# Kernel optimization log

Hardware: AMD Instinct MI355X
Metric: run time of the kernel (lower is better)

## Reference

```python
import jax, jax.numpy as jnp
import numpy as np

EMBED = 2560
HEADS = 8
HEAD_DIM = EMBED // HEADS

def setup_inputs() -> dict:
    key = jax.random.key(0)
    k1, k2, k3, k4, k5 = jax.random.split(key, 5)
    x = jax.random.normal(k1, (2, 2048, EMBED), dtype=jnp.float32)
    # nn.Linear(embed, 3*embed): weight [3E, E], bias [3E]
    s = 1.0 / np.sqrt(EMBED)
    W_qkv = jax.random.uniform(k2, (3 * EMBED, EMBED), jnp.float32, -s, s)
    b_qkv = jax.random.uniform(k3, (3 * EMBED,), jnp.float32, -s, s)
    W_out = jax.random.uniform(k4, (EMBED, EMBED), jnp.float32, -s, s)
    b_out = jax.random.uniform(k5, (EMBED,), jnp.float32, -s, s)
    return {"x": x, "W_qkv": W_qkv, "b_qkv": b_qkv, "W_out": W_out, "b_out": b_out}

def reference(x, W_qkv, b_qkv, W_out, b_out):
    N, S, E = x.shape
    qkv = jnp.einsum('bse,fe->bsf', x, W_qkv) + b_qkv            # [B,S,3E]
    qkv = qkv.reshape(N, S, 3, HEADS, HEAD_DIM)
    q = jnp.transpose(qkv[:, :, 0], (0, 2, 1, 3))                 # [B,H,S,D]
    k = jnp.transpose(qkv[:, :, 1], (0, 2, 1, 3))
    v = jnp.transpose(qkv[:, :, 2], (0, 2, 1, 3))
    scale = jnp.sqrt(jnp.float32(HEAD_DIM))
    attn = jnp.einsum('bhqd,bhkd->bhqk', q, k) / scale            # [B,H,S,S]
    attn = jax.nn.softmax(attn, axis=-1)
    out = jnp.einsum('bhqk,bhkd->bhqd', attn, v)                  # [B,H,S,D]
    out = jnp.transpose(out, (0, 2, 1, 3)).reshape(N, S, E)
    return jnp.einsum('bse,fe->bsf', out, W_out) + b_out
```

## Files before the change

kernel.cpp:

```cpp
#include <hip/hip_runtime.h>

#define EMBED 2560
#define HEADS 8
#define HDIM  320
#define BATCH 2
#define SEQ   2048
#define MTOT  (BATCH*SEQ)
#define FTOT  (3*EMBED)

using bf = __bf16;
typedef __bf16 bf16x8 __attribute__((ext_vector_type(8)));
typedef float  f32x4  __attribute__((ext_vector_type(4)));
typedef short  s16x8  __attribute__((ext_vector_type(8)));
typedef float  f32x4v __attribute__((ext_vector_type(4)));

__device__ __forceinline__ void gl_lds16(const bf* g, bf* l) {
    __builtin_amdgcn_global_load_lds(
        (const __attribute__((address_space(1))) void*)g,
        (__attribute__((address_space(3))) void*)l,
        16, 0, 0);
}

__global__ void cvt_bf16(const float* __restrict__ in, bf* __restrict__ out, int n) {
    int i = (blockIdx.x*blockDim.x + threadIdx.x)*8;
    if (i >= n) return;
    f32x4v a = *reinterpret_cast<const f32x4v*>(in + i);
    f32x4v b = *reinterpret_cast<const f32x4v*>(in + i + 4);
    bf16x8 r;
    r[0]=(bf)a[0]; r[1]=(bf)a[1]; r[2]=(bf)a[2]; r[3]=(bf)a[3];
    r[4]=(bf)b[0]; r[5]=(bf)b[1]; r[6]=(bf)b[2]; r[7]=(bf)b[3];
    *reinterpret_cast<bf16x8*>(out + i) = r;
}

template<bool OUTBF>
__global__ __launch_bounds__(512, 2)
void gemm256(const bf* __restrict__ A, const bf* __restrict__ B,
             const float* __restrict__ bias, void* __restrict__ Cp,
             int M, int N, int K) {
    __shared__ __align__(16) bf AsL[2][2][8192];
    __shared__ __align__(16) bf BsL[2][2][8192];
    const int tid = threadIdx.x, lane = tid & 63, wid = tid >> 6;
    const int wr = wid >> 2, wc = wid & 3;
    const int l15 = lane & 15, l4 = lane >> 4;

    int mb, nb;
    const int i = blockIdx.y*gridDim.x + blockIdx.x;
    if ((gridDim.y == 16) && ((gridDim.x & 1) == 0)) {
        const int xcd = i & 7, j = i >> 3;
        const int pc = xcd & 1, pr = xcd >> 1;
        nb = pc*(gridDim.x >> 1) + (j >> 2);
        mb = pr*4 + (j & 3);
    } else {
        const int nwg = gridDim.x*gridDim.y;
        int bid = ((nwg & 7) == 0) ? (i & 7)*(nwg >> 3) + (i >> 3) : i;
        mb = bid / gridDim.x; nb = bid % gridDim.x;
    }
    const int m0 = mb*256, n0 = nb*256;
    const int NT = K >> 6;

    unsigned aOff[2];
    #pragma unroll
    for (int j = 0; j < 2; ++j) {
        int q = (wid*2 + j)*64 + lane;
        int r = q >> 3, c = q & 7;
        aOff[j] = (unsigned)r*K + (unsigned)((c ^ (r & 7))*8);
    }
    const bf* Ap = A + (size_t)m0*K;
    const bf* Bp = B + (size_t)n0*K;

    auto stA = [&](int bb, int h, int kt) {
        bf* d = &AsL[bb][h][wid*1024];
        const bf* s = Ap + (size_t)h*128*K + (size_t)kt*64;
        gl_lds16(s + aOff[0], d);
        gl_lds16(s + aOff[1], d + 512);
    };
    auto stB = [&](int bb, int h, int kt) {
        bf* d = &BsL[bb][h][wid*1024];
        const bf* s = Bp + (size_t)h*128*K + (size_t)kt*64;
        gl_lds16(s + aOff[0], d);
        gl_lds16(s + aOff[1], d + 512);
    };

    f32x4 acc[8][4] = {};
    bf16x8 aR[4][2], bR0[2][2], bR1[2][2];

    stB(0,0,0); stB(0,1,0); stA(0,0,0); stA(0,1,0); stB(1,0,1); stB(1,1,1);
    asm volatile("s_waitcnt vmcnt(4)" ::: "memory");
    __builtin_amdgcn_s_barrier();

    const int brow0 = (wc & 1)*64;
    for (int kt = 0; kt < NT; ++kt) {
        const int bb = kt & 1;
        const bf* Ab = &AsL[bb][wr][0];
        const bf* Bb = &BsL[bb][wc >> 1][0];

        #pragma unroll
        for (int mi = 0; mi < 4; ++mi)
            #pragma unroll
            for (int kk = 0; kk < 2; ++kk) {
                int r = mi*16 + l15;
                int kg = kk*4 + l4;
                aR[mi][kk] = *reinterpret_cast<const bf16x8*>(&Ab[r*64 + ((kg ^ (r & 7))*8)]);
            }
        #pragma unroll
        for (int ni = 0; ni < 2; ++ni)
            #pragma unroll
            for (int kk = 0; kk < 2; ++kk) {
                int r = brow0 + ni*16 + l15;
                int kg = kk*4 + l4;
                bR0[ni][kk] = *reinterpret_cast<const bf16x8*>(&Bb[r*64 + ((kg ^ (r & 7))*8)]);
            }
        if (kt + 1 < NT) stA(bb^1, 0, kt+1);
        __builtin_amdgcn_s_barrier();
        asm volatile("s_waitcnt lgkmcnt(0)" ::: "memory");
        __builtin_amdgcn_sched_barrier(0);
        __builtin_amdgcn_s_setprio(1);
        #pragma unroll
        for (int mi = 0; mi < 4; ++mi)
            #pragma unroll
            for (int ni = 0; ni < 2; ++ni)
                #pragma unroll
                for (int kk = 0; kk < 2; ++kk)
                    acc[mi][ni] = __builtin_amdgcn_mfma_f32_16x16x32_bf16(aR[mi][kk], bR0[ni][kk], acc[mi][ni], 0, 0, 0);
        __builtin_amdgcn_s_setprio(0);
        __builtin_amdgcn_s_barrier();

        #pragma unroll
        for (int ni = 0; ni < 2; ++ni)
            #pragma unroll
            for (int kk = 0; kk < 2; ++kk) {
                int r = brow0 + 32 + ni*16 + l15;
                int kg = kk*4 + l4;
                bR1[ni][kk] = *reinterpret_cast<const bf16x8*>(&Bb[r*64 + ((kg ^ (r & 7))*8)]);
            }
        if (kt + 1 < NT) stA(bb^1, 1, kt+1);
        __builtin_amdgcn_s_barrier();
        asm volatile("s_waitcnt lgkmcnt(0)" ::: "memory");
        __builtin_amdgcn_sched_barrier(0);
        __builtin_amdgcn_s_setprio(1);
        #pragma unroll
        for (int mi = 0; mi < 4; ++mi)
            #pragma unroll
            for (int ni = 0; ni < 2; ++ni)
                #pragma unroll
                for (int kk = 0; kk < 2; ++kk)
                    acc[mi][2+ni] = __builtin_amdgcn_mfma_f32_16x16x32_bf16(aR[mi][kk], bR1[ni][kk], acc[mi][2+ni], 0, 0, 0);
        __builtin_amdgcn_s_setprio(0);
        __builtin_amdgcn_s_barrier();

        #pragma unroll
        for (int mi = 0; mi < 4; ++mi)
            #pragma unroll
            for (int kk = 0; kk < 2; ++kk) {
                int r = 64 + mi*16 + l15;
                int kg = kk*4 + l4;
                aR[mi][kk] = *reinterpret_cast<const bf16x8*>(&Ab[r*64 + ((kg ^ (r & 7))*8)]);
            }
        if (kt + 2 < NT) stB(bb, 0, kt+2);
        __builtin_amdgcn_s_barrier();
        asm volatile("s_waitcnt lgkmcnt(0)" ::: "memory");
        __builtin_amdgcn_sched_barrier(0);
        __builtin_amdgcn_s_setprio(1);
        #pragma unroll
        for (int mi = 0; mi < 4; ++mi)
            #pragma unroll
            for (int ni = 0; ni < 2; ++ni)
                #pragma unroll
                for (int kk = 0; kk < 2; ++kk)
                    acc[4+mi][2+ni] = __builtin_amdgcn_mfma_f32_16x16x32_bf16(aR[mi][kk], bR1[ni][kk], acc[4+mi][2+ni], 0, 0, 0);
        __builtin_amdgcn_s_setprio(0);
        __builtin_amdgcn_s_barrier();

        if (kt + 2 < NT) stB(bb, 1, kt+2);
        if (kt >= NT-2) asm volatile("s_waitcnt vmcnt(0)" ::: "memory");
        else            asm volatile("s_waitcnt vmcnt(4)" ::: "memory");
        __builtin_amdgcn_s_barrier();
        __builtin_amdgcn_s_setprio(1);
        #pragma unroll
        for (int mi = 0; mi < 4; ++mi)
            #pragma unroll
            for (int ni = 0; ni < 2; ++ni)
                #pragma unroll
                for (int kk = 0; kk < 2; ++kk)
                    acc[4+mi][ni] = __builtin_amdgcn_mfma_f32_16x16x32_bf16(aR[mi][kk], bR0[ni][kk], acc[4+mi][ni], 0, 0, 0);
        __builtin_amdgcn_s_setprio(0);
        __builtin_amdgcn_s_barrier();
    }

    const int cr0 = m0 + wr*128, cc0 = n0 + wc*64;
    #pragma unroll
    for (int NI = 0; NI < 4; ++NI) {
        int colg = cc0 + NI*16 + l15;
        float bv = bias[colg];
        #pragma unroll
        for (int MI = 0; MI < 8; ++MI)
            #pragma unroll
            for (int rr = 0; rr < 4; ++rr) {
                int rowg = cr0 + MI*16 + l4*4 + rr;
                float v = acc[MI][NI][rr] + bv;
                if (OUTBF) ((bf*)Cp)[(size_t)rowg*N + colg] = (bf)v;
                else       ((float*)Cp)[(size_t)rowg*N + colg] = v;
            }
    }
}

__global__ void repack_vt(const bf* __restrict__ qkv, bf* __restrict__ vt) {
    __shared__ bf tile[64][72];
    const int bh = blockIdx.z, b = bh >> 3, h = bh & 7;
    const int s0 = blockIdx.x*64, d0 = blockIdx.y*64;
    const int t = threadIdx.x;
    #pragma unroll
    for (int p = 0; p < 2; ++p) {
        int sr = (t >> 3) + p*32, ck = t & 7;
        s16x8 v = *reinterpret_cast<const s16x8*>(
            qkv + ((size_t)(b*SEQ + s0 + sr))*FTOT + 2*EMBED + h*HDIM + d0 + ck*8);
        *reinterpret_cast<s16x8*>(&tile[sr][ck*8]) = v;
    }
    __syncthreads();
    #pragma unroll
    for (int p = 0; p < 2; ++p) {
        int dr = (t >> 3) + p*32, ck = t & 7;
        bf16x8 r;
        #pragma unroll
        for (int j = 0; j < 8; ++j) r[j] = tile[ck*8 + j][dr];
        *reinterpret_cast<bf16x8*>(vt + ((size_t)bh*HDIM + d0 + dr)*SEQ + s0 + ck*8) = r;
    }
}

__global__ __launch_bounds__(512, 2)
void attn_fwd(const bf* __restrict__ qkv, const bf* __restrict__ vt, bf* __restrict__ aout) {
    __shared__ bf Kls[2][32*320];
    __shared__ bf Vls[2][320*32];
    __shared__ bf Ps[8][16][40];
    const int bh = blockIdx.y, b = bh >> 3, h = bh & 7;
    const int tid = threadIdx.x, lane = tid & 63, wid = tid >> 6;
    const int qw = blockIdx.x*128 + wid*16;
    const int l15 = lane & 15, l4 = lane >> 4;
    const float scale = 0.05590169944f;

    const bf* gsrc[5];
    int ldsoff[5];
    size_t step;
    if (wid < 4) {
        step = (size_t)32*FTOT;
        #pragma unroll
        for (int i = 0; i < 5; ++i) {
            int g = wid*5 + i;
            int q = g*64 + lane;
            int r = q/40, cl = q - r*40;
            int cg = cl ^ (r & 7);
            gsrc[i] = qkv + (size_t)(b*SEQ + r)*FTOT + EMBED + h*HDIM + cg*8;
            ldsoff[i] = g*512;
        }
    } else {
        step = 32;
        #pragma unroll
        for (int i = 0; i < 5; ++i) {
            int g = wid*5 + i - 20;
            int q = g*64 + lane;
            int row = q >> 2, cl = q & 3;
            int cg = cl ^ ((row >> 1) & 3);
            gsrc[i] = vt + (size_t)bh*HDIM*SEQ + (size_t)row*SEQ + cg*8;
            ldsoff[i] = g*512;
        }
    }

    bf16x8 qf[10];
    const bf* qbase = qkv + ((size_t)(b*SEQ + qw + l15))*FTOT + h*HDIM + l4*8;
    #pragma unroll
    for (int d = 0; d < 10; ++d) qf[d] = *reinterpret_cast<const bf16x8*>(qbase + d*32);

    f32x4 o[20] = {};
    float mrow[4], lsum[4];
    #pragma unroll
    for (int r = 0; r < 4; ++r) { mrow[r] = -1e30f; lsum[r] = 0.f; }

    const int r7  = l15 & 7;
    const int vsw = (l4 ^ ((l15 >> 1) & 3))*8;

    {
        bf* lb = (wid < 4) ? &Kls[0][0] : &Vls[0][0];
        #pragma unroll
        for (int i = 0; i < 5; ++i) { gl_lds16(gsrc[i], lb + ldsoff[i]); gsrc[i] += step; }
    }
    __syncthreads();

    for (int kt = 0; kt < SEQ/32; ++kt) {
        const int bb = kt & 1;
        if (kt + 1 < SEQ/32) {
            bf* lb = (wid < 4) ? &Kls[bb^1][0] : &Vls[bb^1][0];
            #pragma unroll
            for (int i = 0; i < 5; ++i) { gl_lds16(gsrc[i], lb + ldsoff[i]); gsrc[i] += step; }
        }
        const bf* Kb = &Kls[bb][0];
        const bf* Vb = &Vls[bb][0];

        f32x4 sc[2] = {};
        #pragma unroll
        for (int kb = 0; kb < 2; ++kb) {
            const int Rbase = (kb*16 + l15)*320;
            #pragma unroll
            for (int d = 0; d < 10; ++d) {
                int c = (d*4 + l4) ^ r7;
                bf16x8 kf = *reinterpret_cast<const bf16x8*>(&Kb[Rbase + c*8]);
                sc[kb] = __builtin_amdgcn_mfma_f32_16x16x32_bf16(qf[d], kf, sc[kb], 0, 0, 0);
            }
        }

        float tmax[4];
        bool need = false;
        #pragma unroll
        for (int r = 0; r < 4; ++r) {
            float v = fmaxf(sc[0][r], sc[1][r])*scale;
            v = fmaxf(v, __shfl_xor(v, 1));
            v = fmaxf(v, __shfl_xor(v, 2));
            v = fmaxf(v, __shfl_xor(v, 4));
            v = fmaxf(v, __shfl_xor(v, 8));
            tmax[r] = v;
            need = need || (v > mrow[r] + 8.f);
        }
        if (__any(need)) {
            float alpha[4];
            #pragma unroll
            for (int r = 0; r < 4; ++r) {
                float nm = fmaxf(mrow[r], tmax[r]);
                alpha[r] = __expf(mrow[r] - nm);
                mrow[r] = nm;
                lsum[r] *= alpha[r];
            }
            #pragma unroll
            for (int c = 0; c < 20; ++c)
                #pragma unroll
                for (int r = 0; r < 4; ++r) o[c][r] *= alpha[r];
        }

        float ps[2][4];
        #pragma unroll
        for (int r = 0; r < 4; ++r) {
            float p0 = __expf(sc[0][r]*scale - mrow[r]);
            float p1 = __expf(sc[1][r]*scale - mrow[r]);
            ps[0][r] = p0; ps[1][r] = p1;
            lsum[r] += p0 + p1;
        }

        #pragma unroll
        for (int kb = 0; kb < 2; ++kb)
            #pragma unroll
            for (int r = 0; r < 4; ++r)
                Ps[wid][l4*4 + r][kb*16 + l15] = (bf)ps[kb][r];

        bf16x8 pf = *reinterpret_cast<const bf16x8*>(&Ps[wid][l15][l4*8]);
        #pragma unroll
        for (int c = 0; c < 20; ++c) {
            bf16x8 vf = *reinterpret_cast<const bf16x8*>(&Vb[(c*16 + l15)*32 + vsw]);
            o[c] = __builtin_amdgcn_mfma_f32_16x16x32_bf16(pf, vf, o[c], 0, 0, 0);
        }
        __syncthreads();
    }

    float inv[4];
    #pragma unroll
    for (int r = 0; r < 4; ++r) {
        float s = lsum[r];
        s += __shfl_xor(s, 1);
        s += __shfl_xor(s, 2);
        s += __shfl_xor(s, 4);
        s += __shfl_xor(s, 8);
        inv[r] = 1.f/s;
    }
    #pragma unroll
    for (int c = 0; c < 20; ++c)
        #pragma unroll
        for (int r = 0; r < 4; ++r) {
            size_t idx = ((size_t)(b*SEQ + qw + l4*4 + r))*EMBED + h*HDIM + c*16 + l15;
            aout[idx] = (bf)(o[c][r]*inv[r]);
        }
}

extern "C" void kernel_launch(void* const* d_in, const int* in_sizes, int n_in,
                              void* d_out, int out_size, void* d_ws, size_t ws_size,
                              hipStream_t stream) {
    const float* x    = (const float*)d_in[0];
    const float* Wqkv = (const float*)d_in[1];
    const float* bqkv = (const float*)d_in[2];
    const float* Wout = (const float*)d_in[3];
    const float* bout = (const float*)d_in[4];
    float* out = (float*)d_out;

    char* ws = (char*)d_ws;
    bf* xb    = (bf*)(ws);
    bf* wqkvb = (bf*)(ws + 20971520);
    bf* woutb = (bf*)(ws + 60293120);
    bf* qkvb  = (bf*)(ws + 73400320);
    bf* vtb   = (bf*)(ws + 136314880);
    bf* attnb = xb;

    cvt_bf16<<<5120, 256, 0, stream>>>(x,    xb,    MTOT*EMBED);
    cvt_bf16<<<9600, 256, 0, stream>>>(Wqkv, wqkvb, FTOT*EMBED);
    cvt_bf16<<<3200, 256, 0, stream>>>(Wout, woutb, EMBED*EMBED);

    gemm256<true ><<<dim3(FTOT/256,  MTOT/256), 512, 0, stream>>>(xb, wqkvb, bqkv, qkvb, MTOT, FTOT, EMBED);
    repack_vt<<<dim3(SEQ/64, HDIM/64, BATCH*HEADS), 256, 0, stream>>>(qkvb, vtb);
    attn_fwd<<<dim3(SEQ/128, BATCH*HEADS), 512, 0, stream>>>(qkvb, vtb, attnb);
    gemm256<false><<<dim3(EMBED/256, MTOT/256), 512, 0, stream>>>(attnb, woutb, bout, out, MTOT, EMBED, EMBED);
}
```

Measured before the change: 427.4 us.

## Shrink attention blocks to 64 queries, drop K/V double buffering, remap blocks per XCD

Attention blocks shrink from 512 threads covering 128 queries to 256 threads covering 64 queries, which doubles the grid to 512 blocks so more CUs are busy. K/V tiles are now single-buffered with a blocking vmcnt wait and barrier each iteration, which halves LDS use but exposes load latency that the prefetch used to hide. Block indices are remapped so each XCD handles two (batch, head) pairs, keeping their K/V in that XCD's L2. Each K/V tile is now read by twice as many blocks, so global traffic rises.

```diff
diff --git a/kernel.cpp b/kernel.cpp
--- a/kernel.cpp
+++ b/kernel.cpp
@@ -227,41 +227,44 @@
     }
 }
 
-__global__ __launch_bounds__(512, 2)
+__global__ __launch_bounds__(256, 2)
 void attn_fwd(const bf* __restrict__ qkv, const bf* __restrict__ vt, bf* __restrict__ aout) {
-    __shared__ bf Kls[2][32*320];
-    __shared__ bf Vls[2][320*32];
-    __shared__ bf Ps[8][16][40];
-    const int bh = blockIdx.y, b = bh >> 3, h = bh & 7;
+    __shared__ bf Ks[32*320];
+    __shared__ bf Vs[320*32];
+    __shared__ bf Ps[4][16][40];
+    const int li = blockIdx.y*gridDim.x + blockIdx.x;
+    const int xcd = li & 7, j = li >> 3;
+    const int bh = 2*xcd + (j >> 5), qt = j & 31;
+    const int b = bh >> 3, h = bh & 7;
     const int tid = threadIdx.x, lane = tid & 63, wid = tid >> 6;
-    const int qw = blockIdx.x*128 + wid*16;
+    const int qw = qt*64 + wid*16;
     const int l15 = lane & 15, l4 = lane >> 4;
     const float scale = 0.05590169944f;
 
-    const bf* gsrc[5];
-    int ldsoff[5];
+    const bf* gsrc[10];
+    int ldsbase;
     size_t step;
-    if (wid < 4) {
+    if (wid < 2) {
         step = (size_t)32*FTOT;
-        #pragma unroll
-        for (int i = 0; i < 5; ++i) {
-            int g = wid*5 + i;
+        ldsbase = wid*10*512;
+        #pragma unroll
+        for (int i = 0; i < 10; ++i) {
+            int g = wid*10 + i;
             int q = g*64 + lane;
             int r = q/40, cl = q - r*40;
             int cg = cl ^ (r & 7);
             gsrc[i] = qkv + (size_t)(b*SEQ + r)*FTOT + EMBED + h*HDIM + cg*8;
-            ldsoff[i] = g*512;
         }
     } else {
         step = 32;
-        #pragma unroll
-        for (int i = 0; i < 5; ++i) {
-            int g = wid*5 + i - 20;
+        ldsbase = (wid-2)*10*512;
+        #pragma unroll
+        for (int i = 0; i < 10; ++i) {
+            int g = (wid-2)*10 + i;
             int q = g*64 + lane;
             int row = q >> 2, cl = q & 3;
             int cg = cl ^ ((row >> 1) & 3);
             gsrc[i] = vt + (size_t)bh*HDIM*SEQ + (size_t)row*SEQ + cg*8;
-            ldsoff[i] = g*512;
         }
     }
 
@@ -278,22 +281,12 @@
     const int r7  = l15 & 7;
     const int vsw = (l4 ^ ((l15 >> 1) & 3))*8;
 
-    {
-        bf* lb = (wid < 4) ? &Kls[0][0] : &Vls[0][0];
-        #pragma unroll
-        for (int i = 0; i < 5; ++i) { gl_lds16(gsrc[i], lb + ldsoff[i]); gsrc[i] += step; }
-    }
-    __syncthreads();
-
     for (int kt = 0; kt < SEQ/32; ++kt) {
-        const int bb = kt & 1;
-        if (kt + 1 < SEQ/32) {
-            bf* lb = (wid < 4) ? &Kls[bb^1][0] : &Vls[bb^1][0];
-            #pragma unroll
-            for (int i = 0; i < 5; ++i) { gl_lds16(gsrc[i], lb + ldsoff[i]); gsrc[i] += step; }
-        }
-        const bf* Kb = &Kls[bb][0];
-        const bf* Vb = &Vls[bb][0];
+        bf* lb = (wid < 2) ? Ks : Vs;
+        #pragma unroll
+        for (int i = 0; i < 10; ++i) { gl_lds16(gsrc[i], lb + ldsbase + i*512); gsrc[i] += step; }
+        asm volatile("s_waitcnt vmcnt(0)" ::: "memory");
+        __syncthreads();
 
         f32x4 sc[2] = {};
         #pragma unroll
@@ -302,7 +295,7 @@
             #pragma unroll
             for (int d = 0; d < 10; ++d) {
                 int c = (d*4 + l4) ^ r7;
-                bf16x8 kf = *reinterpret_cast<const bf16x8*>(&Kb[Rbase + c*8]);
+                bf16x8 kf = *reinterpret_cast<const bf16x8*>(&Ks[Rbase + c*8]);
                 sc[kb] = __builtin_amdgcn_mfma_f32_16x16x32_bf16(qf[d], kf, sc[kb], 0, 0, 0);
             }
         }
@@ -352,7 +345,7 @@
         bf16x8 pf = *reinterpret_cast<const bf16x8*>(&Ps[wid][l15][l4*8]);
         #pragma unroll
         for (int c = 0; c < 20; ++c) {
-            bf16x8 vf = *reinterpret_cast<const bf16x8*>(&Vb[(c*16 + l15)*32 + vsw]);
+            bf16x8 vf = *reinterpret_cast<const bf16x8*>(&Vs[(c*16 + l15)*32 + vsw]);
             o[c] = __builtin_amdgcn_mfma_f32_16x16x32_bf16(pf, vf, o[c], 0, 0, 0);
         }
         __syncthreads();
@@ -401,6 +394,6 @@
 
     gemm256<true ><<<dim3(FTOT/256,  MTOT/256), 512, 0, stream>>>(xb, wqkvb, bqkv, qkvb, MTOT, FTOT, EMBED);
     repack_vt<<<dim3(SEQ/64, HDIM/64, BATCH*HEADS), 256, 0, stream>>>(qkvb, vtb);
-    attn_fwd<<<dim3(SEQ/128, BATCH*HEADS), 512, 0, stream>>>(qkvb, vtb, attnb);
+    attn_fwd<<<dim3(32, 16), 256, 0, stream>>>(qkvb, vtb, attnb);
     gemm256<false><<<dim3(EMBED/256, MTOT/256), 512, 0, stream>>>(attnb, woutb, bout, out, MTOT, EMBED, EMBED);
 }
```

Result: no change. 435.0 us (+1.8%).

## Fuse V transpose into attention loads and merge bf16 conversion kernels

Applied to the files above, without the earlier changes.

Removes the separate repack_vt kernel. Attention V-loading warps now gather V directly from the qkv buffer with strided scalar loads, hold it in registers, and write it transposed into LDS partway through the iteration. The three fp32-to-bf16 conversion launches are also merged into one grid-stride kernel. This saves two launches and one intermediate round trip to global memory. In exchange, the V loads become 2-byte strided gathers instead of 16-byte direct-to-LDS loads, and register pressure rises in the attention loop.

```diff
diff --git a/kernel.cpp b/kernel.cpp
--- a/kernel.cpp
+++ b/kernel.cpp
@@ -21,15 +21,23 @@
         16, 0, 0);
 }
 
-__global__ void cvt_bf16(const float* __restrict__ in, bf* __restrict__ out, int n) {
-    int i = (blockIdx.x*blockDim.x + threadIdx.x)*8;
-    if (i >= n) return;
-    f32x4v a = *reinterpret_cast<const f32x4v*>(in + i);
-    f32x4v b = *reinterpret_cast<const f32x4v*>(in + i + 4);
-    bf16x8 r;
-    r[0]=(bf)a[0]; r[1]=(bf)a[1]; r[2]=(bf)a[2]; r[3]=(bf)a[3];
-    r[4]=(bf)b[0]; r[5]=(bf)b[1]; r[6]=(bf)b[2]; r[7]=(bf)b[3];
-    *reinterpret_cast<bf16x8*>(out + i) = r;
+__global__ void cvt_all(const float* __restrict__ x, const float* __restrict__ wq,
+                        const float* __restrict__ wo, bf* __restrict__ xb,
+                        bf* __restrict__ wqb, bf* __restrict__ wob) {
+    const int N1 = MTOT*EMBED/8, N2 = FTOT*EMBED/8, N3 = EMBED*EMBED/8;
+    const int stride = gridDim.x*blockDim.x;
+    for (int c = blockIdx.x*blockDim.x + threadIdx.x; c < N1+N2+N3; c += stride) {
+        const float* s; bf* d; int o = c;
+        if (c < N1)           { s = x;  d = xb;  }
+        else if (c < N1+N2)   { s = wq; d = wqb; o = c - N1; }
+        else                  { s = wo; d = wob; o = c - N1 - N2; }
+        f32x4v a = *reinterpret_cast<const f32x4v*>(s + (size_t)o*8);
+        f32x4v b = *reinterpret_cast<const f32x4v*>(s + (size_t)o*8 + 4);
+        bf16x8 r;
+        r[0]=(bf)a[0]; r[1]=(bf)a[1]; r[2]=(bf)a[2]; r[3]=(bf)a[3];
+        r[4]=(bf)b[0]; r[5]=(bf)b[1]; r[6]=(bf)b[2]; r[7]=(bf)b[3];
+        *reinterpret_cast<bf16x8*>(d + (size_t)o*8) = r;
+    }
 }
 
 template<bool OUTBF>
@@ -204,31 +212,8 @@
     }
 }
 
-__global__ void repack_vt(const bf* __restrict__ qkv, bf* __restrict__ vt) {
-    __shared__ bf tile[64][72];
-    const int bh = blockIdx.z, b = bh >> 3, h = bh & 7;
-    const int s0 = blockIdx.x*64, d0 = blockIdx.y*64;
-    const int t = threadIdx.x;
-    #pragma unroll
-    for (int p = 0; p < 2; ++p) {
-        int sr = (t >> 3) + p*32, ck = t & 7;
-        s16x8 v = *reinterpret_cast<const s16x8*>(
-            qkv + ((size_t)(b*SEQ + s0 + sr))*FTOT + 2*EMBED + h*HDIM + d0 + ck*8);
-        *reinterpret_cast<s16x8*>(&tile[sr][ck*8]) = v;
-    }
-    __syncthreads();
-    #pragma unroll
-    for (int p = 0; p < 2; ++p) {
-        int dr = (t >> 3) + p*32, ck = t & 7;
-        bf16x8 r;
-        #pragma unroll
-        for (int j = 0; j < 8; ++j) r[j] = tile[ck*8 + j][dr];
-        *reinterpret_cast<bf16x8*>(vt + ((size_t)bh*HDIM + d0 + dr)*SEQ + s0 + ck*8) = r;
-    }
-}
-
 __global__ __launch_bounds__(512, 2)
-void attn_fwd(const bf* __restrict__ qkv, const bf* __restrict__ vt, bf* __restrict__ aout) {
+void attn_fwd(const bf* __restrict__ qkv, bf* __restrict__ aout) {
     __shared__ bf Kls[2][32*320];
     __shared__ bf Vls[2][320*32];
     __shared__ bf Ps[8][16][40];
@@ -240,9 +225,8 @@
 
     const bf* gsrc[5];
     int ldsoff[5];
-    size_t step;
+    const size_t step = (size_t)32*FTOT;
     if (wid < 4) {
-        step = (size_t)32*FTOT;
         #pragma unroll
         for (int i = 0; i < 5; ++i) {
             int g = wid*5 + i;
@@ -253,15 +237,14 @@
             ldsoff[i] = g*512;
         }
     } else {
-        step = 32;
         #pragma unroll
         for (int i = 0; i < 5; ++i) {
             int g = wid*5 + i - 20;
             int q = g*64 + lane;
             int row = q >> 2, cl = q & 3;
             int cg = cl ^ ((row >> 1) & 3);
-            gsrc[i] = vt + (size_t)bh*HDIM*SEQ + (size_t)row*SEQ + cg*8;
-            ldsoff[i] = g*512;
+            gsrc[i] = qkv + (size_t)(b*SEQ + cg*8)*FTOT + 2*EMBED + h*HDIM + row;
+            ldsoff[i] = row*32 + cl*8;
         }
     }
 
@@ -278,19 +261,39 @@
     const int r7  = l15 & 7;
     const int vsw = (l4 ^ ((l15 >> 1) & 3))*8;
 
-    {
-        bf* lb = (wid < 4) ? &Kls[0][0] : &Vls[0][0];
-        #pragma unroll
-        for (int i = 0; i < 5; ++i) { gl_lds16(gsrc[i], lb + ldsoff[i]); gsrc[i] += step; }
+    if (wid < 4) {
+        #pragma unroll
+        for (int i = 0; i < 5; ++i) { gl_lds16(gsrc[i], &Kls[0][0] + ldsoff[i]); gsrc[i] += step; }
+    } else {
+        bf16x8 vr[5];
+        #pragma unroll
+        for (int i = 0; i < 5; ++i)
+            #pragma unroll
+            for (int j = 0; j < 8; ++j) vr[i][j] = gsrc[i][(size_t)j*FTOT];
+        #pragma unroll
+        for (int i = 0; i < 5; ++i) {
+            *reinterpret_cast<bf16x8*>(&Vls[0][0] + ldsoff[i]) = vr[i];
+            gsrc[i] += step;
+        }
     }
     __syncthreads();
 
     for (int kt = 0; kt < SEQ/32; ++kt) {
         const int bb = kt & 1;
-        if (kt + 1 < SEQ/32) {
-            bf* lb = (wid < 4) ? &Kls[bb^1][0] : &Vls[bb^1][0];
-            #pragma unroll
-            for (int i = 0; i < 5; ++i) { gl_lds16(gsrc[i], lb + ldsoff[i]); gsrc[i] += step; }
+        const bool pf = (kt + 1 < SEQ/32);
+        bf16x8 vr[5];
+        if (wid < 4) {
+            if (pf) {
+                #pragma unroll
+                for (int i = 0; i < 5; ++i) { gl_lds16(gsrc[i], &Kls[bb^1][0] + ldsoff[i]); gsrc[i] += step; }
+            }
+        } else if (pf) {
+            #pragma unroll
+            for (int i = 0; i < 5; ++i)
+                #pragma unroll
+                for (int j = 0; j < 8; ++j) vr[i][j] = gsrc[i][(size_t)j*FTOT];
+            #pragma unroll
+            for (int i = 0; i < 5; ++i) gsrc[i] += step;
         }
         const bf* Kb = &Kls[bb][0];
         const bf* Vb = &Vls[bb][0];
@@ -349,11 +352,17 @@
             for (int r = 0; r < 4; ++r)
                 Ps[wid][l4*4 + r][kb*16 + l15] = (bf)ps[kb][r];
 
-        bf16x8 pf = *reinterpret_cast<const bf16x8*>(&Ps[wid][l15][l4*8]);
+        if (wid >= 4 && pf) {
+            #pragma unroll
+            for (int i = 0; i < 5; ++i)
+                *reinterpret_cast<bf16x8*>(&Vls[bb^1][0] + ldsoff[i]) = vr[i];
+        }
+
+        bf16x8 pfrag = *reinterpret_cast<const bf16x8*>(&Ps[wid][l15][l4*8]);
         #pragma unroll
         for (int c = 0; c < 20; ++c) {
             bf16x8 vf = *reinterpret_cast<const bf16x8*>(&Vb[(c*16 + l15)*32 + vsw]);
-            o[c] = __builtin_amdgcn_mfma_f32_16x16x32_bf16(pf, vf, o[c], 0, 0, 0);
+            o[c] = __builtin_amdgcn_mfma_f32_16x16x32_bf16(pfrag, vf, o[c], 0, 0, 0);
         }
         __syncthreads();
     }
@@ -392,15 +401,10 @@
     bf* wqkvb = (bf*)(ws + 20971520);
     bf* woutb = (bf*)(ws + 60293120);
     bf* qkvb  = (bf*)(ws + 73400320);
-    bf* vtb   = (bf*)(ws + 136314880);
     bf* attnb = xb;
 
-    cvt_bf16<<<5120, 256, 0, stream>>>(x,    xb,    MTOT*EMBED);
-    cvt_bf16<<<9600, 256, 0, stream>>>(Wqkv, wqkvb, FTOT*EMBED);
-    cvt_bf16<<<3200, 256, 0, stream>>>(Wout, woutb, EMBED*EMBED);
-
+    cvt_all<<<2048, 256, 0, stream>>>(x, Wqkv, Wout, xb, wqkvb, woutb);
     gemm256<true ><<<dim3(FTOT/256,  MTOT/256), 512, 0, stream>>>(xb, wqkvb, bqkv, qkvb, MTOT, FTOT, EMBED);
-    repack_vt<<<dim3(SEQ/64, HDIM/64, BATCH*HEADS), 256, 0, stream>>>(qkvb, vtb);
-    attn_fwd<<<dim3(SEQ/128, BATCH*HEADS), 512, 0, stream>>>(qkvb, vtb, attnb);
+    attn_fwd<<<dim3(SEQ/128, BATCH*HEADS), 512, 0, stream>>>(qkvb, attnb);
     gemm256<false><<<dim3(EMBED/256, MTOT/256), 512, 0, stream>>>(attnb, woutb, bout, out, MTOT, EMBED, EMBED);
 }
```

New measurement: 533.1 us. 24.7% more time.
